# Performance work log

Hardware: AMD Instinct MI355X
Metric: run time of the kernel (lower is better)

The kernel has to match this reference:

```python
import jax, jax.numpy as jnp
import numpy as np

# --- static config (from init_kwargs) ---
PC_RANGE = np.array([-51.2, -51.2, -5.0, 51.2, 51.2, 3.0], np.float32)
VOXEL_SIZE = np.array([0.2, 0.2, 8.0], np.float32)
GRID = np.round((PC_RANGE[3:] - PC_RANGE[:3]) / VOXEL_SIZE).astype(np.int64)  # [512,512,1]
GX, GY, GZ = int(GRID[0]), int(GRID[1]), int(GRID[2])
GTOT = GX * GY * GZ  # sentinel linear id for invalid points
MAXV = 30000   # max_voxels_num
MAXP = 20      # max_points_in_voxel
NORM_DIMS = np.array([0, 1, 2], np.int32)
B, N, C = 4, 300000, 5


def _voxelize_one(pts):
    """Hard voxelization of one point cloud [N, C] -> (feat [MAXV,MAXP,C], coors [MAXV,3] (zyx), npts [MAXV])."""
    pc_min = jnp.asarray(PC_RANGE[:3], pts.dtype)
    vsize = jnp.asarray(VOXEL_SIZE, pts.dtype)
    coords = jnp.floor((pts[:, :3] - pc_min) / vsize).astype(jnp.int32)  # [N,3] xyz
    grid = jnp.array([GX, GY, GZ], jnp.int32)
    inb = jnp.all((coords >= 0) & (coords < grid), axis=1)
    lin = coords[:, 2] * (GY * GX) + coords[:, 1] * GX + coords[:, 0]
    lin = jnp.where(inb, lin, GTOT)  # invalid points sort to the end
    order = jnp.argsort(lin)  # stable sort -> deterministic assignment
    lin_s, pts_s, coords_s = lin[order], pts[order], coords[order]
    n = pts.shape[0]
    new = jnp.concatenate([jnp.ones((1,), bool), lin_s[1:] != lin_s[:-1]])
    slot = jnp.cumsum(new.astype(jnp.int32)) - 1           # voxel slot (order of first appearance)
    idx = jnp.arange(n, dtype=jnp.int32)
    run_start = jax.lax.cummax(jnp.where(new, idx, 0))     # start index of each voxel run
    rank = idx - run_start                                  # point rank inside its voxel
    keep = (lin_s < GTOT) & (slot < MAXV) & (rank < MAXP)
    slot_s = jnp.where(keep, slot, MAXV)                    # out-of-range -> dropped by scatter
    rank_s = jnp.where(keep, rank, 0)
    feat = jnp.zeros((MAXV, MAXP, pts.shape[1]), pts.dtype).at[slot_s, rank_s].set(pts_s, mode='drop')
    coors = jnp.full((MAXV, 3), -1, jnp.int32).at[slot_s].set(coords_s[:, ::-1], mode='drop')  # zyx
    npts = jnp.zeros((MAXV,), jnp.int32).at[slot_s].add(keep.astype(jnp.int32), mode='drop')
    return feat, coors, npts


def setup_inputs() -> dict:
    key = jax.random.key(0)
    k1, _ = jax.random.split(key)
    u = jax.random.uniform(k1, (B, N, C), dtype=jnp.float32)
    lo = jnp.array([-51.2, -51.2, -5.0, 0.0, 0.0], jnp.float32)
    hi = jnp.array([51.2, 51.2, 3.0, 1.0, 1.0], jnp.float32)
    points = lo + u * (hi - lo)
    norm_range = jnp.asarray(PC_RANGE)
    return {"points": points, "norm_range": norm_range}


def reference(points, norm_range):
    bs = points.shape[0]
    feat, coors, npts = jax.vmap(_voxelize_one)(points)
    feat = feat.reshape(bs * MAXV, MAXP, C)
    npts = npts.reshape(bs * MAXV)
    bidx = jnp.repeat(jnp.arange(bs, dtype=jnp.int32), MAXV)[:, None]
    coors_batch = jnp.concatenate([bidx, coors.reshape(bs * MAXV, 3)], axis=1)  # [B*MAXV, 4]
    # per-dim range normalization: (f - start) / (max - min) on NORM_DIMS only
    dims = jnp.asarray(NORM_DIMS)
    half = norm_range.shape[0] // 2
    start = jnp.zeros((C,), feat.dtype).at[dims].set(norm_range[:half])
    scale = jnp.ones((C,), feat.dtype).at[dims].set(norm_range[half:] - norm_range[:half])
    f = (feat - start) / scale
    # padding-indicator mask
    mask = (jnp.arange(MAXP)[None, :] < npts[:, None]).astype(f.dtype)
    f = f * mask[:, :, None]
    # unsqueeze(0).permute(0, 3, 2, 1) -> [1, C, MAXP, B*MAXV]
    features = jnp.transpose(f[None], (0, 3, 2, 1))
    return features, coors_batch
```

## Files before the change

### kernel.cpp

```cpp
#include <hip/hip_runtime.h>
#include <stdint.h>

typedef unsigned long long u64;
typedef uint32_t u32;
typedef unsigned char u8;

#define B_ 4
#define N_ 300000
#define C_ 5
#define GX_ 512
#define GY_ 512
#define GZ_ 1
#define GTOT_ (GX_*GY_*GZ_)
#define NW_ (GTOT_/64)
#define MAXV_ 30000
#define MAXP_ 20
#define ROWS_ (B_*MAXV_)
#define OUT0_ELEMS_ (C_*MAXP_*ROWS_)

__device__ __forceinline__ int voxel_lin(float x, float y, float z) {
    float qx = (x + 51.2f) * 5.0f;
    float qy = (y + 51.2f) * 5.0f;
    float qz = (z + 5.0f) * 0.125f;
    int cx = (int)floorf(qx);
    int cy = (int)floorf(qy);
    int cz = (int)floorf(qz);
    if (cx < 0 || cx >= GX_ || cy < 0 || cy >= GY_ || cz < 0 || cz >= GZ_) return -1;
    return (cz * GY_ + cy) * GX_ + cx;
}

__global__ void k_init(uint4* __restrict__ occF4) {
    int i = blockIdx.x * blockDim.x + threadIdx.x;
    occF4[i] = make_uint4(0u, 0u, 0u, 0u);
}

__global__ void k_mark(const float* __restrict__ pts, u8* __restrict__ occF) {
    int i = blockIdx.x * blockDim.x + threadIdx.x;
    int b = blockIdx.y;
    if (i >= N_) return;
    const float* p = pts + ((size_t)b * N_ + i) * C_;
    int lin = voxel_lin(p[0], p[1], p[2]);
    if (lin >= 0) occF[(size_t)b * GTOT_ + lin] = (u8)1;
}

__global__ __launch_bounds__(1024) void k_scan(const u8* __restrict__ occF,
                                               u64* __restrict__ occ,
                                               u32* __restrict__ wordOff,
                                               u32* __restrict__ nOcc) {
    int b = blockIdx.x;
    int t = threadIdx.x;
    const u64* of = (const u64*)(occF + (size_t)b * GTOT_);
    int base = t * 4;
    u32 c[4];
    #pragma unroll
    for (int w = 0; w < 4; ++w) {
        const u64* ch = of + (size_t)(base + w) * 8;
        u64 m = 0;
        #pragma unroll
        for (int k = 0; k < 8; ++k) {
            u64 v = ch[k] & 0x0101010101010101ull;
            m |= ((v * 0x0102040810204080ull) >> 56) << (8 * k);
        }
        occ[(size_t)b * NW_ + base + w] = m;
        c[w] = (u32)__popcll(m);
    }
    __shared__ u32 sh[1024];
    sh[t] = c[0] + c[1] + c[2] + c[3];
    __syncthreads();
    for (int off = 1; off < 1024; off <<= 1) {
        u32 v = (t >= off) ? sh[t - off] : 0u;
        __syncthreads();
        sh[t] += v;
        __syncthreads();
    }
    u32 excl = (t > 0) ? sh[t - 1] : 0u;
    u32* wo = wordOff + (size_t)b * NW_ + base;
    wo[0] = excl;
    wo[1] = excl + c[0];
    wo[2] = excl + c[0] + c[1];
    wo[3] = excl + c[0] + c[1] + c[2];
    if (t == 1023) nOcc[b] = sh[1023];
}

__global__ void k_fill(const u64* __restrict__ occ, const u32* __restrict__ wordOff,
                       u32* __restrict__ voxOf, u32* __restrict__ cnt2) {
    int i = blockIdx.x * blockDim.x + threadIdx.x;
    int b = blockIdx.y;
    int w = i >> 6, bit = i & 63;
    u64 m = occ[(size_t)b * NW_ + w];
    if (!((m >> bit) & 1ull)) return;
    u32 slot = wordOff[(size_t)b * NW_ + w] + (u32)__popcll(m & ((1ull << bit) - 1ull));
    if (slot < MAXV_) {
        voxOf[b * MAXV_ + slot] = (u32)i;
        cnt2[b * MAXV_ + slot] = 0u;
    }
}

__global__ void k_scatter(const float* __restrict__ pts, const u64* __restrict__ occ,
                          const u32* __restrict__ wordOff,
                          u32* __restrict__ cnt2, u32* __restrict__ idxbuf) {
    int i = blockIdx.x * blockDim.x + threadIdx.x;
    int b = blockIdx.y;
    if (i >= N_) return;
    const float* p = pts + ((size_t)b * N_ + i) * C_;
    int lin = voxel_lin(p[0], p[1], p[2]);
    if (lin < 0) return;
    int w = lin >> 6, bit = lin & 63;
    u64 m = occ[(size_t)b * NW_ + w];
    u32 slot = wordOff[(size_t)b * NW_ + w] + (u32)__popcll(m & ((1ull << bit) - 1ull));
    if (slot >= MAXV_) return;
    u32 r = atomicAdd(&cnt2[b * MAXV_ + slot], 1u);
    if (r < MAXP_) idxbuf[((size_t)b * MAXV_ + slot) * MAXP_ + r] = (u32)i;
}

__global__ void k_out(const float* __restrict__ pts, const float* __restrict__ nr,
                      const u32* __restrict__ voxOf, const u32* __restrict__ cnt2,
                      const u32* __restrict__ idxbuf, const u32* __restrict__ nOcc,
                      float* __restrict__ out0, float* __restrict__ out1) {
    int row = blockIdx.x * blockDim.x + threadIdx.x;
    if (row >= ROWS_) return;
    int b = row / MAXV_;
    int local = row - b * MAXV_;
    u32 nv = nOcc[b];
    bool valid = (u32)local < (nv < MAXV_ ? nv : (u32)MAXV_);
    u32 lin = 0;
    int n = 0;
    u32 idxs[MAXP_];
    if (valid) {
        lin = voxOf[row];
        n = (int)min(cnt2[row], (u32)MAXP_);
        for (int r = 0; r < n; ++r) idxs[r] = idxbuf[(size_t)row * MAXP_ + r];
        for (int a = 1; a < n; ++a) {
            u32 key = idxs[a];
            int j = a - 1;
            while (j >= 0 && idxs[j] > key) { idxs[j + 1] = idxs[j]; --j; }
            idxs[j + 1] = key;
        }
    }
    float4 cr;
    cr.x = (float)b;
    if (valid) {
        int x = lin & (GX_ - 1);
        int y = (lin >> 9) & (GY_ - 1);
        int z = (int)(lin >> 18);
        cr.y = (float)z; cr.z = (float)y; cr.w = (float)x;
    } else {
        cr.y = -1.0f; cr.z = -1.0f; cr.w = -1.0f;
    }
    *(float4*)(out1 + (size_t)row * 4) = cr;
    float s0 = nr[0], s1 = nr[1], s2 = nr[2];
    float d0 = nr[3] - nr[0], d1 = nr[4] - nr[1], d2 = nr[5] - nr[2];
    for (int p = 0; p < MAXP_; ++p) {
        float f0 = 0.f, f1 = 0.f, f2 = 0.f, f3 = 0.f, f4 = 0.f;
        if (p < n) {
            const float* pp = pts + ((size_t)b * N_ + idxs[p]) * C_;
            f0 = (pp[0] - s0) / d0;
            f1 = (pp[1] - s1) / d1;
            f2 = (pp[2] - s2) / d2;
            f3 = pp[3];
            f4 = pp[4];
        }
        out0[(0 * MAXP_ + p) * ROWS_ + row] = f0;
        out0[(1 * MAXP_ + p) * ROWS_ + row] = f1;
        out0[(2 * MAXP_ + p) * ROWS_ + row] = f2;
        out0[(3 * MAXP_ + p) * ROWS_ + row] = f3;
        out0[(4 * MAXP_ + p) * ROWS_ + row] = f4;
    }
}

extern "C" void kernel_launch(void* const* d_in, const int* in_sizes, int n_in,
                              void* d_out, int out_size, void* d_ws, size_t ws_size,
                              hipStream_t stream) {
    const float* pts = (const float*)d_in[0];
    const float* nr  = (const float*)d_in[1];
    float* out0 = (float*)d_out;
    float* out1 = out0 + (size_t)OUT0_ELEMS_;

    uint8_t* ws = (uint8_t*)d_ws;
    u64* occ     = (u64*)(ws + 0);
    u32* wordOff = (u32*)(ws + 131072);
    u32* voxOf   = (u32*)(ws + 196608);
    u32* cnt2    = (u32*)(ws + 676608);
    u32* idxbuf  = (u32*)(ws + 1156608);
    u32* nOcc    = (u32*)(ws + 10756608);
    u8*  occF    = (u8*)(ws + 1156608);

    dim3 gP((N_ + 255) / 256, B_);
    dim3 gV(GTOT_ / 256, B_);
    k_init   <<<(B_ * GTOT_ / 16 + 255) / 256, 256, 0, stream>>>((uint4*)occF);
    k_mark   <<<gP, 256, 0, stream>>>(pts, occF);
    k_scan   <<<B_, 1024, 0, stream>>>(occF, occ, wordOff, nOcc);
    k_fill   <<<gV, 256, 0, stream>>>(occ, wordOff, voxOf, cnt2);
    k_scatter<<<gP, 256, 0, stream>>>(pts, occ, wordOff, cnt2, idxbuf);
    k_out    <<<(ROWS_ + 255) / 256, 256, 0, stream>>>(pts, nr, voxOf, cnt2, idxbuf, nOcc, out0, out1);
}
```

Baseline: 64.66 us.

## Fuse voxel slot fill into scan and cache per-point voxel ids

The k_fill kernel is removed. The scan kernel now writes voxOf and clears cnt2 directly, walking the set bits of each occupancy word it already holds in registers. k_mark stores each point's linear voxel id in a workspace buffer, so k_scatter reads one int per point instead of re-reading three floats and recomputing the voxel index. k_scatter also returns early when a word's base offset already exceeds MAXV. This saves a launch and a full-grid pass, but it puts a serial bit loop inside a kernel that runs only 4 blocks, and it adds a write and read of a 4.8 MB id buffer.

```diff
diff --git a/kernel.cpp b/kernel.cpp
--- a/kernel.cpp
+++ b/kernel.cpp
@@ -34,23 +34,28 @@
     occF4[i] = make_uint4(0u, 0u, 0u, 0u);
 }
 
-__global__ void k_mark(const float* __restrict__ pts, u8* __restrict__ occF) {
+__global__ void k_mark(const float* __restrict__ pts, u8* __restrict__ occF,
+                       int* __restrict__ linb) {
     int i = blockIdx.x * blockDim.x + threadIdx.x;
     int b = blockIdx.y;
     if (i >= N_) return;
     const float* p = pts + ((size_t)b * N_ + i) * C_;
     int lin = voxel_lin(p[0], p[1], p[2]);
+    linb[(size_t)b * N_ + i] = lin;
     if (lin >= 0) occF[(size_t)b * GTOT_ + lin] = (u8)1;
 }
 
 __global__ __launch_bounds__(1024) void k_scan(const u8* __restrict__ occF,
                                                u64* __restrict__ occ,
                                                u32* __restrict__ wordOff,
+                                               u32* __restrict__ voxOf,
+                                               u32* __restrict__ cnt2,
                                                u32* __restrict__ nOcc) {
     int b = blockIdx.x;
     int t = threadIdx.x;
     const u64* of = (const u64*)(occF + (size_t)b * GTOT_);
     int base = t * 4;
+    u64 msk[4];
     u32 c[4];
     #pragma unroll
     for (int w = 0; w < 4; ++w) {
@@ -62,6 +67,7 @@
             m |= ((v * 0x0102040810204080ull) >> 56) << (8 * k);
         }
         occ[(size_t)b * NW_ + base + w] = m;
+        msk[w] = m;
         c[w] = (u32)__popcll(m);
     }
     __shared__ u32 sh[1024];
@@ -74,40 +80,44 @@
         __syncthreads();
     }
     u32 excl = (t > 0) ? sh[t - 1] : 0u;
-    u32* wo = wordOff + (size_t)b * NW_ + base;
+    u32 wo[4];
     wo[0] = excl;
     wo[1] = excl + c[0];
     wo[2] = excl + c[0] + c[1];
     wo[3] = excl + c[0] + c[1] + c[2];
+    u32* wop = wordOff + (size_t)b * NW_ + base;
+    wop[0] = wo[0]; wop[1] = wo[1]; wop[2] = wo[2]; wop[3] = wo[3];
     if (t == 1023) nOcc[b] = sh[1023];
-}
-
-__global__ void k_fill(const u64* __restrict__ occ, const u32* __restrict__ wordOff,
-                       u32* __restrict__ voxOf, u32* __restrict__ cnt2) {
-    int i = blockIdx.x * blockDim.x + threadIdx.x;
-    int b = blockIdx.y;
-    int w = i >> 6, bit = i & 63;
-    u64 m = occ[(size_t)b * NW_ + w];
-    if (!((m >> bit) & 1ull)) return;
-    u32 slot = wordOff[(size_t)b * NW_ + w] + (u32)__popcll(m & ((1ull << bit) - 1ull));
-    if (slot < MAXV_) {
-        voxOf[b * MAXV_ + slot] = (u32)i;
-        cnt2[b * MAXV_ + slot] = 0u;
-    }
-}
-
-__global__ void k_scatter(const float* __restrict__ pts, const u64* __restrict__ occ,
+    #pragma unroll
+    for (int w = 0; w < 4; ++w) {
+        u32 off = wo[w];
+        if (off >= MAXV_) break;
+        u64 m = msk[w];
+        int vbase = (base + w) << 6;
+        while (m) {
+            int bit = (int)__ffsll((unsigned long long)m) - 1;
+            m &= m - 1;
+            if (off >= MAXV_) break;
+            voxOf[b * MAXV_ + off] = (u32)(vbase + bit);
+            cnt2[b * MAXV_ + off] = 0u;
+            ++off;
+        }
+    }
+}
+
+__global__ void k_scatter(const int* __restrict__ linb, const u64* __restrict__ occ,
                           const u32* __restrict__ wordOff,
                           u32* __restrict__ cnt2, u32* __restrict__ idxbuf) {
     int i = blockIdx.x * blockDim.x + threadIdx.x;
     int b = blockIdx.y;
     if (i >= N_) return;
-    const float* p = pts + ((size_t)b * N_ + i) * C_;
-    int lin = voxel_lin(p[0], p[1], p[2]);
+    int lin = linb[(size_t)b * N_ + i];
     if (lin < 0) return;
     int w = lin >> 6, bit = lin & 63;
+    u32 baseOff = wordOff[(size_t)b * NW_ + w];
+    if (baseOff >= MAXV_) return;
     u64 m = occ[(size_t)b * NW_ + w];
-    u32 slot = wordOff[(size_t)b * NW_ + w] + (u32)__popcll(m & ((1ull << bit) - 1ull));
+    u32 slot = baseOff + (u32)__popcll(m & ((1ull << bit) - 1ull));
     if (slot >= MAXV_) return;
     u32 r = atomicAdd(&cnt2[b * MAXV_ + slot], 1u);
     if (r < MAXP_) idxbuf[((size_t)b * MAXV_ + slot) * MAXP_ + r] = (u32)i;
@@ -182,15 +192,14 @@
     u32* voxOf   = (u32*)(ws + 196608);
     u32* cnt2    = (u32*)(ws + 676608);
     u32* idxbuf  = (u32*)(ws + 1156608);
-    u32* nOcc    = (u32*)(ws + 10756608);
+    int* linb    = (int*)(ws + 10756608);
+    u32* nOcc    = (u32*)(ws + 15556608);
     u8*  occF    = (u8*)(ws + 1156608);
 
     dim3 gP((N_ + 255) / 256, B_);
-    dim3 gV(GTOT_ / 256, B_);
     k_init   <<<(B_ * GTOT_ / 16 + 255) / 256, 256, 0, stream>>>((uint4*)occF);
-    k_mark   <<<gP, 256, 0, stream>>>(pts, occF);
-    k_scan   <<<B_, 1024, 0, stream>>>(occF, occ, wordOff, nOcc);
-    k_fill   <<<gV, 256, 0, stream>>>(occ, wordOff, voxOf, cnt2);
-    k_scatter<<<gP, 256, 0, stream>>>(pts, occ, wordOff, cnt2, idxbuf);
+    k_mark   <<<gP, 256, 0, stream>>>(pts, occF, linb);
+    k_scan   <<<B_, 1024, 0, stream>>>(occF, occ, wordOff, voxOf, cnt2, nOcc);
+    k_scatter<<<gP, 256, 0, stream>>>(linb, occ, wordOff, cnt2, idxbuf);
     k_out    <<<(ROWS_ + 255) / 256, 256, 0, stream>>>(pts, nr, voxOf, cnt2, idxbuf, nOcc, out0, out1);
 }
```

After: 94.13 us. 45.6% more time.

## Parallelize occupancy bitmask build and cache per-point voxel ids

Applied to the files above, without the earlier changes.

The single-block-per-batch scan, which read the whole 256K-byte occupancy flag array with only 4 blocks, is split in two. A wide ballot-based kernel first builds the bitmask words and their popcounts, and a light scan then works only on the word counts. The mark pass now stores each point's linear voxel id, so the scatter pass reads 4 bytes per point instead of re-reading the strided xyz floats and recomputing. Scatter also exits early when a word's base offset already exceeds MAXV. The cost is one extra launch and an extra 4.8MB write plus read of the voxel id buffer.

```diff
diff --git a/kernel.cpp b/kernel.cpp
--- a/kernel.cpp
+++ b/kernel.cpp
@@ -34,51 +34,52 @@
     occF4[i] = make_uint4(0u, 0u, 0u, 0u);
 }
 
-__global__ void k_mark(const float* __restrict__ pts, u8* __restrict__ occF) {
+__global__ void k_mark(const float* __restrict__ pts, u8* __restrict__ occF,
+                       int* __restrict__ linb) {
     int i = blockIdx.x * blockDim.x + threadIdx.x;
     int b = blockIdx.y;
     if (i >= N_) return;
     const float* p = pts + ((size_t)b * N_ + i) * C_;
     int lin = voxel_lin(p[0], p[1], p[2]);
+    linb[(size_t)b * N_ + i] = lin;
     if (lin >= 0) occF[(size_t)b * GTOT_ + lin] = (u8)1;
 }
 
-__global__ __launch_bounds__(1024) void k_scan(const u8* __restrict__ occF,
-                                               u64* __restrict__ occ,
-                                               u32* __restrict__ wordOff,
-                                               u32* __restrict__ nOcc) {
+__global__ void k_maskcnt(const u8* __restrict__ occF, u64* __restrict__ occ,
+                          u32* __restrict__ wordPop) {
+    int i = blockIdx.x * blockDim.x + threadIdx.x;
+    int b = blockIdx.y;
+    u8 f = occF[(size_t)b * GTOT_ + i];
+    u64 m = __ballot(f != 0);
+    if ((threadIdx.x & 63) == 0) {
+        int w = i >> 6;
+        occ[(size_t)b * NW_ + w] = m;
+        wordPop[(size_t)b * NW_ + w] = (u32)__popcll(m);
+    }
+}
+
+__global__ __launch_bounds__(1024) void k_scan2(const u32* __restrict__ wordPop,
+                                                u32* __restrict__ wordOff,
+                                                u32* __restrict__ nOcc) {
     int b = blockIdx.x;
     int t = threadIdx.x;
-    const u64* of = (const u64*)(occF + (size_t)b * GTOT_);
-    int base = t * 4;
-    u32 c[4];
-    #pragma unroll
-    for (int w = 0; w < 4; ++w) {
-        const u64* ch = of + (size_t)(base + w) * 8;
-        u64 m = 0;
-        #pragma unroll
-        for (int k = 0; k < 8; ++k) {
-            u64 v = ch[k] & 0x0101010101010101ull;
-            m |= ((v * 0x0102040810204080ull) >> 56) << (8 * k);
-        }
-        occ[(size_t)b * NW_ + base + w] = m;
-        c[w] = (u32)__popcll(m);
-    }
+    const uint4* wp = (const uint4*)(wordPop + (size_t)b * NW_);
+    uint4 v = wp[t];
     __shared__ u32 sh[1024];
-    sh[t] = c[0] + c[1] + c[2] + c[3];
+    sh[t] = v.x + v.y + v.z + v.w;
     __syncthreads();
     for (int off = 1; off < 1024; off <<= 1) {
-        u32 v = (t >= off) ? sh[t - off] : 0u;
+        u32 u = (t >= off) ? sh[t - off] : 0u;
         __syncthreads();
-        sh[t] += v;
+        sh[t] += u;
         __syncthreads();
     }
     u32 excl = (t > 0) ? sh[t - 1] : 0u;
-    u32* wo = wordOff + (size_t)b * NW_ + base;
+    u32* wo = wordOff + (size_t)b * NW_ + t * 4;
     wo[0] = excl;
-    wo[1] = excl + c[0];
-    wo[2] = excl + c[0] + c[1];
-    wo[3] = excl + c[0] + c[1] + c[2];
+    wo[1] = excl + v.x;
+    wo[2] = excl + v.x + v.y;
+    wo[3] = excl + v.x + v.y + v.z;
     if (t == 1023) nOcc[b] = sh[1023];
 }
 
@@ -96,18 +97,19 @@
     }
 }
 
-__global__ void k_scatter(const float* __restrict__ pts, const u64* __restrict__ occ,
+__global__ void k_scatter(const int* __restrict__ linb, const u64* __restrict__ occ,
                           const u32* __restrict__ wordOff,
                           u32* __restrict__ cnt2, u32* __restrict__ idxbuf) {
     int i = blockIdx.x * blockDim.x + threadIdx.x;
     int b = blockIdx.y;
     if (i >= N_) return;
-    const float* p = pts + ((size_t)b * N_ + i) * C_;
-    int lin = voxel_lin(p[0], p[1], p[2]);
+    int lin = linb[(size_t)b * N_ + i];
     if (lin < 0) return;
     int w = lin >> 6, bit = lin & 63;
+    u32 baseOff = wordOff[(size_t)b * NW_ + w];
+    if (baseOff >= MAXV_) return;
     u64 m = occ[(size_t)b * NW_ + w];
-    u32 slot = wordOff[(size_t)b * NW_ + w] + (u32)__popcll(m & ((1ull << bit) - 1ull));
+    u32 slot = baseOff + (u32)__popcll(m & ((1ull << bit) - 1ull));
     if (slot >= MAXV_) return;
     u32 r = atomicAdd(&cnt2[b * MAXV_ + slot], 1u);
     if (r < MAXP_) idxbuf[((size_t)b * MAXV_ + slot) * MAXP_ + r] = (u32)i;
@@ -182,15 +184,18 @@
     u32* voxOf   = (u32*)(ws + 196608);
     u32* cnt2    = (u32*)(ws + 676608);
     u32* idxbuf  = (u32*)(ws + 1156608);
-    u32* nOcc    = (u32*)(ws + 10756608);
+    int* linb    = (int*)(ws + 10756608);
+    u32* wordPop = (u32*)(ws + 15556608);
+    u32* nOcc    = (u32*)(ws + 15622144);
     u8*  occF    = (u8*)(ws + 1156608);
 
     dim3 gP((N_ + 255) / 256, B_);
     dim3 gV(GTOT_ / 256, B_);
     k_init   <<<(B_ * GTOT_ / 16 + 255) / 256, 256, 0, stream>>>((uint4*)occF);
-    k_mark   <<<gP, 256, 0, stream>>>(pts, occF);
-    k_scan   <<<B_, 1024, 0, stream>>>(occF, occ, wordOff, nOcc);
+    k_mark   <<<gP, 256, 0, stream>>>(pts, occF, linb);
+    k_maskcnt<<<gV, 256, 0, stream>>>(occF, occ, wordPop);
+    k_scan2  <<<B_, 1024, 0, stream>>>(wordPop, wordOff, nOcc);
     k_fill   <<<gV, 256, 0, stream>>>(occ, wordOff, voxOf, cnt2);
-    k_scatter<<<gP, 256, 0, stream>>>(pts, occ, wordOff, cnt2, idxbuf);
+    k_scatter<<<gP, 256, 0, stream>>>(linb, occ, wordOff, cnt2, idxbuf);
     k_out    <<<(ROWS_ + 255) / 256, 256, 0, stream>>>(pts, nr, voxOf, cnt2, idxbuf, nOcc, out0, out1);
 }
```

Result: faster. 58.95 us (-8.8%).
